# Kernel tuning notes

Measured on AMD Instinct MI355X. Metric: run time of the kernel, lower is better.

The kernel has to match this reference:

```python
import jax, jax.numpy as jnp
import numpy as np

FP8_E4M3_MAX = 448.0  # max finite value of float8_e4m3fn
SCALE = 2.0          # input activation scale
WEIGHT_SCALE = 2.0   # weight scale
IN_FEATURES = 4096
OUT_FEATURES = 4096
M = 4096


def setup_inputs() -> dict:
    key = jax.random.key(0)
    k_in, k_w, k_b = jax.random.split(key, 3)
    inp = jax.random.normal(k_in, (M, IN_FEATURES), dtype=jnp.float32)
    # weight is stored in fp8 e4m3fn in the module; materialize the fp8-quantized
    # values (cast randn -> fp8 -> back) so float32 array holds exact fp8 grid values
    w_raw = jax.random.normal(k_w, (OUT_FEATURES, IN_FEATURES), dtype=jnp.float32)
    weight = w_raw.astype(jnp.float8_e4m3fn).astype(jnp.float32)
    bias = jax.random.normal(k_b, (OUT_FEATURES,), dtype=jnp.float32)
    return {"input": inp, "weight": weight, "bias": bias}


def _quant_dequant_fp8(x, scale):
    # quantize_affine_float8: clamp(x/scale) to fp8 range, cast to e4m3fn;
    # dequantize: cast back to float and multiply by scale
    q = jnp.clip(x / scale, -FP8_E4M3_MAX, FP8_E4M3_MAX).astype(jnp.float8_e4m3fn)
    return q.astype(jnp.float32) * scale


def reference(input, weight, bias):
    # dequantize fp8 weight (values already on fp8 grid): w_fp32 = w * weight_scale
    w_dq = weight * WEIGHT_SCALE                     # [out, in]
    dq_input = _quant_dequant_fp8(input, SCALE)      # [M, in]
    out = jnp.einsum("mi,oi->mo", dq_input, w_dq)    # fp32 GEMM
    return out + bias
```

## Files before the change

### kernel.cpp

```cpp
#include <hip/hip_runtime.h>
#include <hip/hip_bf16.h>
#include <stdint.h>


typedef __attribute__((ext_vector_type(4))) float f32x4;
typedef __attribute__((ext_vector_type(2))) int i32x2;
typedef __attribute__((ext_vector_type(4))) int i32x4;
typedef __attribute__((ext_vector_type(8))) int i32x8;

#define FP8_MAX 448.0f
#define UNIT_SCALE 0x7F7F7F7F

__global__ void quant_fp8_kernel(const float* __restrict__ x,
                                 uint32_t* __restrict__ q,
                                 float mul, int n8) {
    int i = blockIdx.x * blockDim.x + threadIdx.x;
    if (i >= n8) return;
    const float4* xv = (const float4*)x;
    float4 v0 = xv[2 * i];
    float4 v1 = xv[2 * i + 1];
    float a[8] = {v0.x, v0.y, v0.z, v0.w, v1.x, v1.y, v1.z, v1.w};
#pragma unroll
    for (int j = 0; j < 8; ++j) {
        float t = a[j] * mul;
        t = fminf(fmaxf(t, -FP8_MAX), FP8_MAX);
        a[j] = t;
    }
    int lo = 0, hi = 0;
    lo = __builtin_amdgcn_cvt_pk_fp8_f32(a[0], a[1], lo, false);
    lo = __builtin_amdgcn_cvt_pk_fp8_f32(a[2], a[3], lo, true);
    hi = __builtin_amdgcn_cvt_pk_fp8_f32(a[4], a[5], hi, false);
    hi = __builtin_amdgcn_cvt_pk_fp8_f32(a[6], a[7], hi, true);
    i32x2 out;
    out.x = lo;
    out.y = hi;
    ((i32x2*)q)[i] = out;
}

#define KTILES 32

__device__ static inline void gload_lds16(const void* g, void* l) {
    __builtin_amdgcn_global_load_lds(
        (const __attribute__((address_space(1))) void*)g,
        (__attribute__((address_space(3))) void*)l, 16, 0, 0);
}

#define STAGE_FULL(GSRC, KB, LBASE)                                        \
    gload_lds16((GSRC) + (KB),       (LBASE) + t * 16);                    \
    gload_lds16((GSRC) + (KB) + 32,  (LBASE) + 8192  + t * 16);            \
    gload_lds16((GSRC) + (KB) + 64,  (LBASE) + 16384 + t * 16);            \
    gload_lds16((GSRC) + (KB) + 96,  (LBASE) + 24576 + t * 16);

#define READ_A(LBASE, MH)                                                  \
    _Pragma("unroll") for (int m = 0; m < 4; ++m) {                        \
        i32x4 lo = *(const i32x4*)((LBASE) + aoff + (MH) * 1024 + m * 256);       \
        i32x4 hi = *(const i32x4*)((LBASE) + aoff + (MH) * 1024 + m * 256 + 4096);\
        areg[m] = (i32x8){lo[0], lo[1], lo[2], lo[3], hi[0], hi[1], hi[2], hi[3]};\
    }

#define READ_B_ALL(LBASE)                                                  \
    _Pragma("unroll") for (int n = 0; n < 4; ++n) {                        \
        i32x4 lo = *(const i32x4*)((LBASE) + boff + n * 256);                     \
        i32x4 hi = *(const i32x4*)((LBASE) + boff + n * 256 + 4096);              \
        breg[n] = (i32x8){lo[0], lo[1], lo[2], lo[3], hi[0], hi[1], hi[2], hi[3]};\
    }

#define MFMA16(MH)                                                         \
    __builtin_amdgcn_s_setprio(1);                                         \
    _Pragma("unroll") for (int m = 0; m < 4; ++m)                          \
        _Pragma("unroll") for (int n = 0; n < 4; ++n)                      \
            acc[(MH) * 4 + m][n] =                                         \
                __builtin_amdgcn_mfma_scale_f32_16x16x128_f8f6f4(          \
                    areg[m], breg[n], acc[(MH) * 4 + m][n],                \
                    0, 0, 0, UNIT_SCALE, 0, UNIT_SCALE);                   \
    __builtin_amdgcn_s_setprio(0);

#define BAR() __builtin_amdgcn_s_barrier()
#define VMW(N) asm volatile("s_waitcnt vmcnt(" #N ")" ::: "memory")

__global__ __launch_bounds__(512, 2) void fp8_gemm_bias_kernel(
        const uint8_t* __restrict__ Aq, const uint8_t* __restrict__ Wq,
        const float* __restrict__ bias, float* __restrict__ C,
        int M, int N, int K) {
    __shared__ __align__(16) uint8_t lds[131072];

    const int t = threadIdx.x;
    const int lane = t & 63;
    const int w = t >> 6;
    const int wr = w >> 2;
    const int wc = w & 3;
    const int lr = lane & 15;
    const int lk = lane >> 4;

    const int bid = blockIdx.x;
    const int swz = (bid & 7) * 32 + (bid >> 3);
    const int bm = swz >> 4;
    const int bn = swz & 15;

    const uint8_t* Abase = Aq + (size_t)(bm * 256) * K;
    const uint8_t* Bbase = Wq + (size_t)(bn * 256) * K;

    const int srow = t & 255;
    const int scol = (t >> 8) * 16;
    const uint8_t* gA = Abase + (size_t)srow * K + scol;
    const uint8_t* gB = Bbase + (size_t)srow * K + scol;

    const int aoff = lk * 8192 + wr * 2048 + lr * 16;
    const int boff = lk * 8192 + wc * 1024 + lr * 16;

    f32x4 acc[8][4];
#pragma unroll
    for (int mi = 0; mi < 8; ++mi)
#pragma unroll
        for (int ni = 0; ni < 4; ++ni)
            acc[mi][ni] = (f32x4){0.f, 0.f, 0.f, 0.f};

    i32x8 areg[4], breg[4];

    STAGE_FULL(gA, 0, lds)
    STAGE_FULL(gB, 0, lds + 32768)
    STAGE_FULL(gB, 128, lds + 98304)
    STAGE_FULL(gA, 128, lds + 65536)
    VMW(8);
    BAR();

    for (int k = 0; k < KTILES; ++k) {
        const int co = (k & 1) << 16;
        uint8_t* const sAc = lds + co;
        uint8_t* const sBc = lds + 32768 + co;
        const int kbN = ((k + 2) & 31) * 128;

        READ_A(sAc, 0)
        READ_B_ALL(sBc)
        BAR();
        MFMA16(0)

        READ_A(sAc, 1)
        STAGE_FULL(gB, kbN, sBc)
        VMW(4);
        BAR();
        STAGE_FULL(gA, kbN, sAc)
        MFMA16(1)
    }

    VMW(0);

    const int crow0 = bm * 256 + wr * 128 + lk * 4;
    const int ccol0 = bn * 256 + wc * 64 + lr;
#pragma unroll
    for (int ni = 0; ni < 4; ++ni) {
        const int col = ccol0 + ni * 16;
        const float bv = bias[col];
#pragma unroll
        for (int mi = 0; mi < 8; ++mi) {
            const int row = crow0 + mi * 16;
#pragma unroll
            for (int j = 0; j < 4; ++j) {
                C[(size_t)(row + j) * N + col] = acc[mi][ni][j] * 4.0f + bv;
            }
        }
    }
}

extern "C" void kernel_launch(void* const* d_in, const int* in_sizes, int n_in,
                              void* d_out, int out_size, void* d_ws, size_t ws_size,
                              hipStream_t stream) {
    const int M = 4096, N = 4096, K = 4096;
    const float* input  = (const float*)d_in[0];
    const float* weight = (const float*)d_in[1];
    const float* bias   = (const float*)d_in[2];
    float* out = (float*)d_out;

    uint8_t* Aq = (uint8_t*)d_ws;
    uint8_t* Wq = (uint8_t*)d_ws + (size_t)M * K;

    {
        int n8 = (M * K) / 8;
        int blocks = (n8 + 255) / 256;
        quant_fp8_kernel<<<blocks, 256, 0, stream>>>(input, (uint32_t*)Aq, 0.5f, n8);
        quant_fp8_kernel<<<blocks, 256, 0, stream>>>(weight, (uint32_t*)Wq, 1.0f, n8);
    }

    dim3 grid(256);
    fp8_gemm_bias_kernel<<<grid, 512, 0, stream>>>(Aq, Wq, bias, out, M, N, K);
}
```

Before: 129.4 us.

## Use 16 waves per block with 4x4 wave grid and halved per-wave tiles

```diff
diff --git a/kernel.cpp b/kernel.cpp
--- a/kernel.cpp
+++ b/kernel.cpp
@@ -45,40 +45,38 @@
         (__attribute__((address_space(3))) void*)l, 16, 0, 0);
 }
 
-#define STAGE_FULL(GSRC, KB, LBASE)                                        \
-    gload_lds16((GSRC) + (KB),       (LBASE) + t * 16);                    \
-    gload_lds16((GSRC) + (KB) + 32,  (LBASE) + 8192  + t * 16);            \
-    gload_lds16((GSRC) + (KB) + 64,  (LBASE) + 16384 + t * 16);            \
-    gload_lds16((GSRC) + (KB) + 96,  (LBASE) + 24576 + t * 16);
+#define STAGE_FULL(GSRC, KB, LBASE)                                       \
+    gload_lds16((GSRC) + (KB),      (LBASE) + t * 16);                    \
+    gload_lds16((GSRC) + (KB) + 64, (LBASE) + 16384 + t * 16);
 
-#define READ_A(LBASE, MH)                                                  \
+#define READ_A_ALL(LBASE)                                                  \
     _Pragma("unroll") for (int m = 0; m < 4; ++m) {                        \
-        i32x4 lo = *(const i32x4*)((LBASE) + aoff + (MH) * 1024 + m * 256);       \
-        i32x4 hi = *(const i32x4*)((LBASE) + aoff + (MH) * 1024 + m * 256 + 4096);\
+        i32x4 lo = *(const i32x4*)((LBASE) + aoff + m * 256);                     \
+        i32x4 hi = *(const i32x4*)((LBASE) + aoff + m * 256 + 4096);              \
         areg[m] = (i32x8){lo[0], lo[1], lo[2], lo[3], hi[0], hi[1], hi[2], hi[3]};\
     }
 
-#define READ_B_ALL(LBASE)                                                  \
-    _Pragma("unroll") for (int n = 0; n < 4; ++n) {                        \
-        i32x4 lo = *(const i32x4*)((LBASE) + boff + n * 256);                     \
-        i32x4 hi = *(const i32x4*)((LBASE) + boff + n * 256 + 4096);              \
+#define READ_B2(LBASE, NH)                                                 \
+    _Pragma("unroll") for (int n = 0; n < 2; ++n) {                        \
+        i32x4 lo = *(const i32x4*)((LBASE) + boff + (NH) * 512 + n * 256);        \
+        i32x4 hi = *(const i32x4*)((LBASE) + boff + (NH) * 512 + n * 256 + 4096); \
         breg[n] = (i32x8){lo[0], lo[1], lo[2], lo[3], hi[0], hi[1], hi[2], hi[3]};\
     }
 
-#define MFMA16(MH)                                                         \
+#define MFMA8(NH)                                                          \
     __builtin_amdgcn_s_setprio(1);                                         \
     _Pragma("unroll") for (int m = 0; m < 4; ++m)                          \
-        _Pragma("unroll") for (int n = 0; n < 4; ++n)                      \
-            acc[(MH) * 4 + m][n] =                                         \
+        _Pragma("unroll") for (int n = 0; n < 2; ++n)                      \
+            acc[m][(NH) * 2 + n] =                                         \
                 __builtin_amdgcn_mfma_scale_f32_16x16x128_f8f6f4(          \
-                    areg[m], breg[n], acc[(MH) * 4 + m][n],                \
+                    areg[m], breg[n], acc[m][(NH) * 2 + n],                \
                     0, 0, 0, UNIT_SCALE, 0, UNIT_SCALE);                   \
     __builtin_amdgcn_s_setprio(0);
 
 #define BAR() __builtin_amdgcn_s_barrier()
 #define VMW(N) asm volatile("s_waitcnt vmcnt(" #N ")" ::: "memory")
 
-__global__ __launch_bounds__(512, 2) void fp8_gemm_bias_kernel(
+__global__ __launch_bounds__(1024) void fp8_gemm_bias_kernel(
         const uint8_t* __restrict__ Aq, const uint8_t* __restrict__ Wq,
         const float* __restrict__ bias, float* __restrict__ C,
         int M, int N, int K) {
@@ -87,8 +85,8 @@
     const int t = threadIdx.x;
     const int lane = t & 63;
     const int w = t >> 6;
-    const int wr = w >> 2;
-    const int wc = w & 3;
+    const int wrow = w >> 2;
+    const int wcol = w & 3;
     const int lr = lane & 15;
     const int lk = lane >> 4;
 
@@ -105,23 +103,23 @@
     const uint8_t* gA = Abase + (size_t)srow * K + scol;
     const uint8_t* gB = Bbase + (size_t)srow * K + scol;
 
-    const int aoff = lk * 8192 + wr * 2048 + lr * 16;
-    const int boff = lk * 8192 + wc * 1024 + lr * 16;
+    const int aoff = lk * 8192 + wrow * 1024 + lr * 16;
+    const int boff = lk * 8192 + wcol * 1024 + lr * 16;
 
-    f32x4 acc[8][4];
+    f32x4 acc[4][4];
 #pragma unroll
-    for (int mi = 0; mi < 8; ++mi)
+    for (int mi = 0; mi < 4; ++mi)
 #pragma unroll
         for (int ni = 0; ni < 4; ++ni)
             acc[mi][ni] = (f32x4){0.f, 0.f, 0.f, 0.f};
 
-    i32x8 areg[4], breg[4];
+    i32x8 areg[4], breg[2];
 
     STAGE_FULL(gA, 0, lds)
     STAGE_FULL(gB, 0, lds + 32768)
     STAGE_FULL(gB, 128, lds + 98304)
     STAGE_FULL(gA, 128, lds + 65536)
-    VMW(8);
+    VMW(4);
     BAR();
 
     for (int k = 0; k < KTILES; ++k) {
@@ -130,29 +128,29 @@
         uint8_t* const sBc = lds + 32768 + co;
         const int kbN = ((k + 2) & 31) * 128;
 
-        READ_A(sAc, 0)
-        READ_B_ALL(sBc)
+        READ_A_ALL(sAc)
+        READ_B2(sBc, 0)
         BAR();
-        MFMA16(0)
+        MFMA8(0)
 
-        READ_A(sAc, 1)
+        READ_B2(sBc, 1)
+        VMW(0);
+        BAR();
         STAGE_FULL(gB, kbN, sBc)
-        VMW(4);
-        BAR();
         STAGE_FULL(gA, kbN, sAc)
-        MFMA16(1)
+        MFMA8(1)
     }
 
     VMW(0);
 
-    const int crow0 = bm * 256 + wr * 128 + lk * 4;
-    const int ccol0 = bn * 256 + wc * 64 + lr;
+    const int crow0 = bm * 256 + wrow * 64 + lk * 4;
+    const int ccol0 = bn * 256 + wcol * 64 + lr;
 #pragma unroll
     for (int ni = 0; ni < 4; ++ni) {
         const int col = ccol0 + ni * 16;
         const float bv = bias[col];
 #pragma unroll
-        for (int mi = 0; mi < 8; ++mi) {
+        for (int mi = 0; mi < 4; ++mi) {
             const int row = crow0 + mi * 16;
 #pragma unroll
             for (int j = 0; j < 4; ++j) {
@@ -182,5 +180,5 @@
     }
 
     dim3 grid(256);
-    fp8_gemm_bias_kernel<<<grid, 512, 0, stream>>>(Aq, Wq, bias, out, M, N, K);
+    fp8_gemm_bias_kernel<<<grid, 1024, 0, stream>>>(Aq, Wq, bias, out, M, N, K);
 }
```

Result: slower. 288.1 us (+122.7%).

## Restructure GEMM main loop into register double-buffered ping-pong pipeline

Applied to the files above, without the earlier changes.

```diff
diff --git a/kernel.cpp b/kernel.cpp
--- a/kernel.cpp
+++ b/kernel.cpp
@@ -45,33 +45,33 @@
         (__attribute__((address_space(3))) void*)l, 16, 0, 0);
 }
 
-#define STAGE_FULL(GSRC, KB, LBASE)                                        \
-    gload_lds16((GSRC) + (KB),       (LBASE) + t * 16);                    \
-    gload_lds16((GSRC) + (KB) + 32,  (LBASE) + 8192  + t * 16);            \
-    gload_lds16((GSRC) + (KB) + 64,  (LBASE) + 16384 + t * 16);            \
-    gload_lds16((GSRC) + (KB) + 96,  (LBASE) + 24576 + t * 16);
-
-#define READ_A(LBASE, MH)                                                  \
+#define STAGE_OP(GSRC, KB, LBASE)                                          \
+    gload_lds16((GSRC) + (KB),      (LBASE) + t * 16);                     \
+    gload_lds16((GSRC) + (KB) + 32, (LBASE) + 8192  + t * 16);             \
+    gload_lds16((GSRC) + (KB) + 64, (LBASE) + 16384 + t * 16);             \
+    gload_lds16((GSRC) + (KB) + 96, (LBASE) + 24576 + t * 16);
+
+#define READ_A(LBASE, MH, DST)                                             \
     _Pragma("unroll") for (int m = 0; m < 4; ++m) {                        \
         i32x4 lo = *(const i32x4*)((LBASE) + aoff + (MH) * 1024 + m * 256);       \
         i32x4 hi = *(const i32x4*)((LBASE) + aoff + (MH) * 1024 + m * 256 + 4096);\
-        areg[m] = (i32x8){lo[0], lo[1], lo[2], lo[3], hi[0], hi[1], hi[2], hi[3]};\
-    }
-
-#define READ_B_ALL(LBASE)                                                  \
+        DST[m] = (i32x8){lo[0], lo[1], lo[2], lo[3], hi[0], hi[1], hi[2], hi[3]}; \
+    }
+
+#define READ_B(LBASE, DST)                                                 \
     _Pragma("unroll") for (int n = 0; n < 4; ++n) {                        \
         i32x4 lo = *(const i32x4*)((LBASE) + boff + n * 256);                     \
         i32x4 hi = *(const i32x4*)((LBASE) + boff + n * 256 + 4096);              \
-        breg[n] = (i32x8){lo[0], lo[1], lo[2], lo[3], hi[0], hi[1], hi[2], hi[3]};\
-    }
-
-#define MFMA16(MH)                                                         \
+        DST[n] = (i32x8){lo[0], lo[1], lo[2], lo[3], hi[0], hi[1], hi[2], hi[3]}; \
+    }
+
+#define MFMA16(AR, BR, MH)                                                 \
     __builtin_amdgcn_s_setprio(1);                                         \
     _Pragma("unroll") for (int m = 0; m < 4; ++m)                          \
         _Pragma("unroll") for (int n = 0; n < 4; ++n)                      \
             acc[(MH) * 4 + m][n] =                                         \
                 __builtin_amdgcn_mfma_scale_f32_16x16x128_f8f6f4(          \
-                    areg[m], breg[n], acc[(MH) * 4 + m][n],                \
+                    AR[m], BR[n], acc[(MH) * 4 + m][n],                    \
                     0, 0, 0, UNIT_SCALE, 0, UNIT_SCALE);                   \
     __builtin_amdgcn_s_setprio(0);
 
@@ -83,6 +83,10 @@
         const float* __restrict__ bias, float* __restrict__ C,
         int M, int N, int K) {
     __shared__ __align__(16) uint8_t lds[131072];
+    uint8_t* const LA0 = lds;
+    uint8_t* const LB0 = lds + 32768;
+    uint8_t* const LA1 = lds + 65536;
+    uint8_t* const LB1 = lds + 98304;
 
     const int t = threadIdx.x;
     const int lane = t & 63;
@@ -115,32 +119,43 @@
         for (int ni = 0; ni < 4; ++ni)
             acc[mi][ni] = (f32x4){0.f, 0.f, 0.f, 0.f};
 
-    i32x8 areg[4], breg[4];
-
-    STAGE_FULL(gA, 0, lds)
-    STAGE_FULL(gB, 0, lds + 32768)
-    STAGE_FULL(gB, 128, lds + 98304)
-    STAGE_FULL(gA, 128, lds + 65536)
-    VMW(8);
+    i32x8 aX[4], aY[4], bE[4], bO[4];
+
+    STAGE_OP(gA, 0, LA0)
+    STAGE_OP(gB, 0, LB0)
+    VMW(0);
     BAR();
-
-    for (int k = 0; k < KTILES; ++k) {
-        const int co = (k & 1) << 16;
-        uint8_t* const sAc = lds + co;
-        uint8_t* const sBc = lds + 32768 + co;
-        const int kbN = ((k + 2) & 31) * 128;
-
-        READ_A(sAc, 0)
-        READ_B_ALL(sBc)
-        BAR();
-        MFMA16(0)
-
-        READ_A(sAc, 1)
-        STAGE_FULL(gB, kbN, sBc)
-        VMW(4);
-        BAR();
-        STAGE_FULL(gA, kbN, sAc)
-        MFMA16(1)
+    READ_A(LA0, 0, aX)
+    READ_B(LB0, bE)
+    STAGE_OP(gA, 128, LA1)
+    STAGE_OP(gB, 128, LB1)
+    BAR();
+
+    for (int kk = 0; kk < KTILES / 2; ++kk) {
+        const int kb2 = ((2 * kk + 2) & 31) * 128;
+        const int kb3 = ((2 * kk + 3) & 31) * 128;
+
+        READ_A(LA0, 1, aY)
+        MFMA16(aX, bE, 0)
+        VMW(0);
+        BAR();
+        READ_A(LA1, 0, aX)
+        READ_B(LB1, bO)
+        STAGE_OP(gA, kb2, LA0)
+        STAGE_OP(gB, kb2, LB0)
+        MFMA16(aY, bE, 1)
+        BAR();
+
+        READ_A(LA1, 1, aY)
+        MFMA16(aX, bO, 0)
+        VMW(0);
+        BAR();
+        READ_A(LA0, 0, aX)
+        READ_B(LB0, bE)
+        STAGE_OP(gA, kb3, LA1)
+        STAGE_OP(gB, kb3, LB1)
+        MFMA16(aY, bO, 1)
+        BAR();
     }
 
     VMW(0);
```

Result: slower. 181.4 us (+40.2%).
